# Kernel optimization log

Hardware: AMD Instinct MI355X
Metric: run time of the kernel (lower is better)

## Reference

```python
import jax, jax.numpy as jnp
import numpy as np

N_NODES = 100000
N_EDGES = 3200000
N_FEAT = 128
H = 16
N_CLASSES = 10


def gcn_conv(x, edge_index, W, b, num_nodes):
    """PyG GCNConv (eval): add self-loops, symmetric norm, linear, scatter-add, bias."""
    xw = x @ W  # [N, out]
    loops = jnp.arange(num_nodes, dtype=edge_index.dtype)
    src = jnp.concatenate([edge_index[0], loops])  # message sources (x_j)
    dst = jnp.concatenate([edge_index[1], loops])  # aggregation targets
    ones = jnp.ones(src.shape[0], dtype=xw.dtype)
    deg = jax.ops.segment_sum(ones, dst, num_segments=num_nodes)
    dinv = jnp.where(deg > 0, jax.lax.rsqrt(deg), 0.0)
    norm = dinv[src] * dinv[dst]  # [E+N]
    msg = xw[src] * norm[:, None]  # gather + scale
    out = jax.ops.segment_sum(msg, dst, num_segments=num_nodes)
    return out + b


def setup_inputs() -> dict:
    key = jax.random.key(0)
    ks = jax.random.split(key, 8)
    x = jax.random.normal(ks[0], (N_NODES, N_FEAT), dtype=jnp.float32)
    edge_index = jax.random.randint(ks[1], (2, N_EDGES), 0, N_NODES, dtype=jnp.int64)
    topo_edges = jax.random.randint(ks[2], (2, N_EDGES), 0, N_NODES, dtype=jnp.int64)
    s1 = 1.0 / np.sqrt(N_FEAT)
    s4 = 1.0 / np.sqrt(2 * H)
    W1 = jax.random.normal(ks[3], (N_FEAT, H), dtype=jnp.float32) * s1
    b1 = jnp.zeros((H,), dtype=jnp.float32)
    W2 = jax.random.normal(ks[4], (N_FEAT, H), dtype=jnp.float32) * s1
    b2 = jnp.zeros((H,), dtype=jnp.float32)
    W4 = jax.random.normal(ks[5], (2 * H, N_CLASSES), dtype=jnp.float32) * s4
    b4 = jnp.zeros((N_CLASSES,), dtype=jnp.float32)
    return {"x": x, "edge_index": edge_index, "topo_edges": topo_edges,
            "W1": W1, "b1": b1, "W2": W2, "b2": b2, "W4": W4, "b4": b4}


def reference(x, edge_index, topo_edges, W1, b1, W2, b2, W4, b4):
    n = x.shape[0]
    # branch 1: structural edges
    x1 = jax.nn.relu(gcn_conv(x, edge_index, W1, b1, n))
    # branch 2: topological edges
    x2 = jax.nn.relu(gcn_conv(x, topo_edges, W2, b2, n))
    # dropout is identity in eval mode
    h = jnp.concatenate([x1, x2], axis=1)  # [N, 2H]
    logits = gcn_conv(h, edge_index, W4, b4, n)  # [N, num_classes]
    return jax.nn.log_softmax(logits, axis=1)
```

## Files before the change

kernel.cpp:

```cpp
#include <hip/hip_runtime.h>
#include <hip/hip_fp16.h>

#define N_NODES 100000
#define N_EDGES 3200000
#define NB 1024
#define BW 98
#define SLOT 4096
#define CHUNK 16384


__global__ void k_zero(int* __restrict__ bcur1, int* __restrict__ bcur2) {
    int i = blockIdx.x * blockDim.x + threadIdx.x;
    if (i < NB) { bcur1[i] = 0; bcur2[i] = 0; }
}

__global__ __launch_bounds__(256) void k_part(const int* __restrict__ ei, const int* __restrict__ te,
                                              int* __restrict__ bcur1, int* __restrict__ bcur2,
                                              unsigned* __restrict__ tmp1, unsigned* __restrict__ tmp2,
                                              int E, int PB) {
    extern __shared__ unsigned smem[];
    unsigned* sorted = smem;
    int* loff = (int*)(smem + CHUNK);
    int* rank = loff + NB;
    int* bas  = rank + NB;
    int* ps   = bas + NB;

    int gb = blockIdx.x;
    bool g2 = gb >= PB;
    const int* ed = g2 ? te : ei;
    int* bcur     = g2 ? bcur2 : bcur1;
    unsigned* tmp = g2 ? tmp2 : tmp1;
    int blk = g2 ? gb - PB : gb;
    int t = threadIdx.x;

    for (int i = t; i < NB; i += 256) rank[i] = 0;
    __syncthreads();
    int base = blk * CHUNK, end = min(base + CHUNK, E);
    int csize = end - base;
    for (int e = base + t; e < end; e += 256) atomicAdd(&rank[ed[E + e] / BW], 1);
    __syncthreads();
    int i4 = t * 4;
    int c0 = rank[i4], c1 = rank[i4 + 1], c2 = rank[i4 + 2], c3 = rank[i4 + 3];
    int tot = c0 + c1 + c2 + c3;
    ps[t] = tot;
    __syncthreads();
    #pragma unroll
    for (int d = 1; d < 256; d <<= 1) {
        int a = (t >= d) ? ps[t - d] : 0;
        __syncthreads();
        ps[t] += a;
        __syncthreads();
    }
    int excl = ps[t] - tot;
    loff[i4]     = excl;
    loff[i4 + 1] = excl + c0;
    loff[i4 + 2] = excl + c0 + c1;
    loff[i4 + 3] = excl + c0 + c1 + c2;
    bas[i4]     = c0 ? atomicAdd(&bcur[i4], c0)     : 0;
    bas[i4 + 1] = c1 ? atomicAdd(&bcur[i4 + 1], c1) : 0;
    bas[i4 + 2] = c2 ? atomicAdd(&bcur[i4 + 2], c2) : 0;
    bas[i4 + 3] = c3 ? atomicAdd(&bcur[i4 + 3], c3) : 0;
    rank[i4] = 0; rank[i4 + 1] = 0; rank[i4 + 2] = 0; rank[i4 + 3] = 0;
    __syncthreads();
    for (int e = base + t; e < end; e += 256) {
        int d = ed[E + e], s = ed[e];
        int b = d / BW;
        int r = atomicAdd(&rank[b], 1);
        sorted[loff[b] + r] = ((unsigned)(d - b * BW) << 20) | (unsigned)s;
    }
    __syncthreads();
    for (int i = t; i < csize; i += 256) {
        int lo = 0, hi = NB - 1;
        while (lo < hi) {
            int mid = (lo + hi + 1) >> 1;
            if (loff[mid] <= i) lo = mid; else hi = mid - 1;
        }
        int b = lo;
        int pos = bas[b] + (i - loff[b]);
        if (pos < SLOT) tmp[(size_t)b * SLOT + pos] = sorted[i];
    }
}

__global__ __launch_bounds__(256) void k_csr(const int* __restrict__ bcur1, const int* __restrict__ bcur2,
                                             unsigned* __restrict__ tmp1, unsigned* __restrict__ tmp2,
                                             int2* __restrict__ pk1, int2* __restrict__ pk2,
                                             float* __restrict__ dinv1, float* __restrict__ dinv2, int n) {
    __shared__ unsigned stage[SLOT];
    __shared__ int ncnt[BW], noff[BW], nrank[BW];
    int gb = blockIdx.x;
    bool g2 = gb >= NB;
    int b = g2 ? gb - NB : gb;
    unsigned* tmp = g2 ? tmp2 : tmp1;
    int2* pk      = g2 ? pk2 : pk1;
    float* dinv   = g2 ? dinv2 : dinv1;
    int sz = min((g2 ? bcur2 : bcur1)[b], SLOT);
    int t = threadIdx.x;
    if (t < BW) { ncnt[t] = 0; nrank[t] = 0; }
    __syncthreads();
    size_t base = (size_t)b * SLOT;
    for (int i = t; i < sz; i += 256) {
        unsigned v = tmp[base + i];
        stage[i] = v;
        atomicAdd(&ncnt[v >> 20], 1);
    }
    __syncthreads();
    if (t == 0) {
        int run = 0;
        for (int k = 0; k < BW; ++k) { noff[k] = run; run += ncnt[k]; }
    }
    __syncthreads();
    int nd = b * BW + t;
    if (t < BW && nd < n) {
        pk[nd] = make_int2((int)base + noff[t], ncnt[t]);
        dinv[nd] = rsqrtf((float)ncnt[t] + 1.f);
    }
    for (int i = t; i < sz; i += 256) {
        unsigned v = stage[i];
        int ld = v >> 20;
        int r = atomicAdd(&nrank[ld], 1);
        tmp[base + noff[ld] + r] = v & 0xFFFFFu;
    }
}

__global__ __launch_bounds__(256) void k_gemm12(
    const float* __restrict__ x,
    const float* __restrict__ W1, const float* __restrict__ W2,
    const float* __restrict__ dinv1, const float* __restrict__ dinv2,
    __half* __restrict__ xwh1, __half* __restrict__ xwh2, int n) {
    __shared__ float Wl[128][32];
    __shared__ float xs[8][128];
    int t = threadIdx.x;
    for (int i = t; i < 128 * 16; i += 256) {
        int k = i / 16, o = i % 16;
        Wl[k][o]      = W1[i];
        Wl[k][o + 16] = W2[i];
    }
    int node0 = blockIdx.x * 8;
    for (int i = t; i < 8 * 128; i += 256) {
        int r = i >> 7, c = i & 127;
        int node = node0 + r;
        xs[r][c] = (node < n) ? x[node * 128 + c] : 0.f;
    }
    __syncthreads();
    int r = t >> 5, o = t & 31;
    int node = node0 + r;
    if (node < n) {
        float s = 0.f;
        #pragma unroll
        for (int k = 0; k < 128; ++k) s += xs[r][k] * Wl[k][o];
        if (o < 16) xwh1[(size_t)node * 16 + o]        = __float2half(s * dinv1[node]);
        else        xwh2[(size_t)node * 16 + (o - 16)] = __float2half(s * dinv2[node]);
    }
}

__global__ __launch_bounds__(256) void k_gather12(
    const __half* __restrict__ xwh1, const __half* __restrict__ xwh2,
    const unsigned* __restrict__ csr1, const unsigned* __restrict__ csr2,
    const int2* __restrict__ pk1, const int2* __restrict__ pk2,
    const float* __restrict__ dinv1, const float* __restrict__ dinv2,
    const float* __restrict__ b1, const float* __restrict__ b2,
    __half* __restrict__ h, int n) {
    int t = threadIdx.x;
    int node = blockIdx.x * 8 + (t >> 5);
    int c = t & 31;
    if (node >= n) return;
    bool g1 = (c < 16);
    int cl = g1 ? c : (c - 16);
    const __half* xw    = g1 ? xwh1 : xwh2;
    const unsigned* csr = g1 ? csr1 : csr2;
    int2 oc = g1 ? pk1[node] : pk2[node];
    int o = oc.x, m = oc.y;
    float di = g1 ? dinv1[node] : dinv2[node];
    float acc = __half2float(xw[(size_t)node * 16 + cl]);
    int k = 0;
    for (; k + 4 <= m; k += 4) {
        unsigned j0 = csr[o + k], j1 = csr[o + k + 1], j2 = csr[o + k + 2], j3 = csr[o + k + 3];
        acc += __half2float(xw[(size_t)j0 * 16 + cl]);
        acc += __half2float(xw[(size_t)j1 * 16 + cl]);
        acc += __half2float(xw[(size_t)j2 * 16 + cl]);
        acc += __half2float(xw[(size_t)j3 * 16 + cl]);
    }
    for (; k < m; ++k) acc += __half2float(xw[(size_t)csr[o + k] * 16 + cl]);
    acc *= di;
    float bv = g1 ? b1[cl] : b2[cl];
    float v = acc + bv;
    h[(size_t)node * 32 + c] = __float2half(v > 0.f ? v : 0.f);
}

__global__ void k_gemm3(const __half* __restrict__ h, const float* __restrict__ W4,
                        const float* __restrict__ dinv1, __half* __restrict__ zsh, int n) {
    int i = blockIdx.x * blockDim.x + threadIdx.x;
    if (i >= n) return;
    float hr[32];
    const __half2* hp = (const __half2*)(h + (size_t)i * 32);
    #pragma unroll
    for (int q = 0; q < 16; ++q) {
        float2 f = __half22float2(hp[q]);
        hr[2 * q] = f.x; hr[2 * q + 1] = f.y;
    }
    float di = dinv1[i];
    #pragma unroll
    for (int c = 0; c < 10; ++c) {
        float s = 0.f;
        #pragma unroll
        for (int k = 0; k < 32; ++k) s += hr[k] * W4[k * 10 + c];
        zsh[(size_t)i * 16 + c] = __float2half(s * di);
    }
}

__global__ __launch_bounds__(256) void k_gather3(
    const __half* __restrict__ zsh,
    const unsigned* __restrict__ csr1, const int2* __restrict__ pk1,
    const float* __restrict__ dinv1,
    const float* __restrict__ b4, float* __restrict__ out, int n) {
    int t = threadIdx.x;
    int node = blockIdx.x * 16 + (t >> 4);
    int c = t & 15;
    if (node >= n) return;
    bool act = (c < 10);
    int cc = act ? c : 0;
    float di = dinv1[node];
    float acc = __half2float(zsh[(size_t)node * 16 + cc]);
    int2 oc = pk1[node];
    int o = oc.x, m = oc.y;
    int k = 0;
    for (; k + 4 <= m; k += 4) {
        unsigned j0 = csr1[o + k], j1 = csr1[o + k + 1], j2 = csr1[o + k + 2], j3 = csr1[o + k + 3];
        acc += __half2float(zsh[(size_t)j0 * 16 + cc]);
        acc += __half2float(zsh[(size_t)j1 * 16 + cc]);
        acc += __half2float(zsh[(size_t)j2 * 16 + cc]);
        acc += __half2float(zsh[(size_t)j3 * 16 + cc]);
    }
    for (; k < m; ++k) acc += __half2float(zsh[(size_t)csr1[o + k] * 16 + cc]);
    float logit = acc * di + b4[cc];
    float mv = act ? logit : -1e30f;
    #pragma unroll
    for (int w = 8; w >= 1; w >>= 1) mv = fmaxf(mv, __shfl_xor(mv, w, 16));
    float ex = act ? expf(logit - mv) : 0.f;
    float ssum = ex;
    #pragma unroll
    for (int w = 8; w >= 1; w >>= 1) ssum += __shfl_xor(ssum, w, 16);
    if (act) out[(size_t)node * 10 + c] = logit - mv - logf(ssum);
}

extern "C" void kernel_launch(void* const* d_in, const int* in_sizes, int n_in,
                              void* d_out, int out_size, void* d_ws, size_t ws_size,
                              hipStream_t stream) {
    const float* x  = (const float*)d_in[0];
    const int*   ei = (const int*)d_in[1];
    const int*   te = (const int*)d_in[2];
    const float* W1 = (const float*)d_in[3];
    const float* b1 = (const float*)d_in[4];
    const float* W2 = (const float*)d_in[5];
    const float* b2 = (const float*)d_in[6];
    const float* W4 = (const float*)d_in[7];
    const float* b4 = (const float*)d_in[8];
    float* out = (float*)d_out;

    const int N = N_NODES, E = N_EDGES;

    char* w = (char*)d_ws;
    auto alloc = [&](size_t bytes) { void* p = (void*)w; w += (bytes + 255) & ~255ull; return p; };
    int*      bcur1 = (int*)alloc((size_t)NB * 4);
    int*      bcur2 = (int*)alloc((size_t)NB * 4);
    int2*     pk1   = (int2*)alloc((size_t)N * 8);
    int2*     pk2   = (int2*)alloc((size_t)N * 8);
    float*    dinv1 = (float*)alloc((size_t)N * 4);
    float*    dinv2 = (float*)alloc((size_t)N * 4);
    unsigned* tmp1  = (unsigned*)alloc((size_t)NB * SLOT * 4);
    unsigned* tmp2  = (unsigned*)alloc((size_t)NB * SLOT * 4);
    __half*   xwh1  = (__half*)alloc((size_t)N * 16 * 2);
    __half*   xwh2  = (__half*)alloc((size_t)N * 16 * 2);
    __half*   h     = (__half*)alloc((size_t)N * 32 * 2);
    __half*   zsh   = (__half*)alloc((size_t)N * 16 * 2);

    const int PB = (E + CHUNK - 1) / CHUNK;
    const size_t PART_LDS = ((size_t)CHUNK + 3 * NB + 256) * 4;
    k_zero<<<(NB + 255) / 256, 256, 0, stream>>>(bcur1, bcur2);
    k_part<<<2 * PB, 256, PART_LDS, stream>>>(ei, te, bcur1, bcur2, tmp1, tmp2, E, PB);
    k_csr<<<2 * NB, 256, 0, stream>>>(bcur1, bcur2, tmp1, tmp2, pk1, pk2, dinv1, dinv2, N);
    k_gemm12<<<(N + 7) / 8, 256, 0, stream>>>(x, W1, W2, dinv1, dinv2, xwh1, xwh2, N);
    k_gather12<<<(N + 7) / 8, 256, 0, stream>>>(xwh1, xwh2, tmp1, tmp2, pk1, pk2,
                                                dinv1, dinv2, b1, b2, h, N);
    k_gemm3<<<(N + 255) / 256, 256, 0, stream>>>(h, W4, dinv1, zsh, N);
    k_gather3<<<(N + 15) / 16, 256, 0, stream>>>(zsh, tmp1, pk1, dinv1, b4, out, N);
}
```

Baseline: 426.0 us.

## Replace atomic bucket slots with deterministic per-chunk offset tables and compact CSR

The partition kernel no longer claims bucket positions with global atomics into fixed 4096-entry slots. Each chunk now writes its locally sorted edges contiguously, along with a per-bucket offset table. A new kernel prefix-sums the per-bucket totals to get global bucket bases, and the CSR kernel gathers each bucket's pieces from every chunk into shared memory before building a compact CSR. This removes the global atomics, the per-element binary search and the sparse slotted layout, at the cost of an extra kernel and many small strided reads in the CSR stage. The k_csr gather loop is sized for at most 256 chunks and, like the old SLOT limit, silently drops edges beyond a bucket capacity (now 4608). It also reuses the tmp buffers for the fp16 activations, and the block size changes to 512.

Result: slower. 443.6 us (+4.1%).

```diff
diff --git a/kernel.cpp b/kernel.cpp
--- a/kernel.cpp
+++ b/kernel.cpp
@@ -5,104 +5,134 @@
 #define N_EDGES 3200000
 #define NB 1024
 #define BW 98
-#define SLOT 4096
+#define TBS (NB + 1)
 #define CHUNK 16384
-
-
-__global__ void k_zero(int* __restrict__ bcur1, int* __restrict__ bcur2) {
-    int i = blockIdx.x * blockDim.x + threadIdx.x;
-    if (i < NB) { bcur1[i] = 0; bcur2[i] = 0; }
-}
-
-__global__ __launch_bounds__(256) void k_part(const int* __restrict__ ei, const int* __restrict__ te,
-                                              int* __restrict__ bcur1, int* __restrict__ bcur2,
+#define STCAP 4608
+
+
+__global__ __launch_bounds__(512) void k_part(const int* __restrict__ ei, const int* __restrict__ te,
                                               unsigned* __restrict__ tmp1, unsigned* __restrict__ tmp2,
+                                              unsigned short* __restrict__ tbl1, unsigned short* __restrict__ tbl2,
                                               int E, int PB) {
     extern __shared__ unsigned smem[];
     unsigned* sorted = smem;
-    int* loff = (int*)(smem + CHUNK);
-    int* rank = loff + NB;
-    int* bas  = rank + NB;
-    int* ps   = bas + NB;
+    int* rank = (int*)(smem + CHUNK);
+    int* loff = rank + NB;
+    int* ps   = loff + NB;
 
     int gb = blockIdx.x;
     bool g2 = gb >= PB;
-    const int* ed = g2 ? te : ei;
-    int* bcur     = g2 ? bcur2 : bcur1;
-    unsigned* tmp = g2 ? tmp2 : tmp1;
+    const int* ed        = g2 ? te : ei;
+    unsigned* tmp        = g2 ? tmp2 : tmp1;
+    unsigned short* tbl  = g2 ? tbl2 : tbl1;
     int blk = g2 ? gb - PB : gb;
     int t = threadIdx.x;
 
-    for (int i = t; i < NB; i += 256) rank[i] = 0;
+    for (int i = t; i < NB; i += 512) rank[i] = 0;
     __syncthreads();
     int base = blk * CHUNK, end = min(base + CHUNK, E);
     int csize = end - base;
-    for (int e = base + t; e < end; e += 256) atomicAdd(&rank[ed[E + e] / BW], 1);
-    __syncthreads();
-    int i4 = t * 4;
-    int c0 = rank[i4], c1 = rank[i4 + 1], c2 = rank[i4 + 2], c3 = rank[i4 + 3];
-    int tot = c0 + c1 + c2 + c3;
+    for (int e = base + t; e < end; e += 512) atomicAdd(&rank[ed[E + e] / BW], 1);
+    __syncthreads();
+    int i2 = t * 2;
+    int c0 = rank[i2], c1 = rank[i2 + 1];
+    int tot = c0 + c1;
     ps[t] = tot;
     __syncthreads();
     #pragma unroll
-    for (int d = 1; d < 256; d <<= 1) {
+    for (int d = 1; d < 512; d <<= 1) {
         int a = (t >= d) ? ps[t - d] : 0;
         __syncthreads();
         ps[t] += a;
         __syncthreads();
     }
     int excl = ps[t] - tot;
-    loff[i4]     = excl;
-    loff[i4 + 1] = excl + c0;
-    loff[i4 + 2] = excl + c0 + c1;
-    loff[i4 + 3] = excl + c0 + c1 + c2;
-    bas[i4]     = c0 ? atomicAdd(&bcur[i4], c0)     : 0;
-    bas[i4 + 1] = c1 ? atomicAdd(&bcur[i4 + 1], c1) : 0;
-    bas[i4 + 2] = c2 ? atomicAdd(&bcur[i4 + 2], c2) : 0;
-    bas[i4 + 3] = c3 ? atomicAdd(&bcur[i4 + 3], c3) : 0;
-    rank[i4] = 0; rank[i4 + 1] = 0; rank[i4 + 2] = 0; rank[i4 + 3] = 0;
-    __syncthreads();
-    for (int e = base + t; e < end; e += 256) {
+    loff[i2]     = excl;
+    loff[i2 + 1] = excl + c0;
+    rank[i2] = 0; rank[i2 + 1] = 0;
+    __syncthreads();
+    for (int e = base + t; e < end; e += 512) {
         int d = ed[E + e], s = ed[e];
         int b = d / BW;
         int r = atomicAdd(&rank[b], 1);
         sorted[loff[b] + r] = ((unsigned)(d - b * BW) << 20) | (unsigned)s;
     }
     __syncthreads();
-    for (int i = t; i < csize; i += 256) {
-        int lo = 0, hi = NB - 1;
-        while (lo < hi) {
-            int mid = (lo + hi + 1) >> 1;
-            if (loff[mid] <= i) lo = mid; else hi = mid - 1;
-        }
-        int b = lo;
-        int pos = bas[b] + (i - loff[b]);
-        if (pos < SLOT) tmp[(size_t)b * SLOT + pos] = sorted[i];
-    }
-}
-
-__global__ __launch_bounds__(256) void k_csr(const int* __restrict__ bcur1, const int* __restrict__ bcur2,
-                                             unsigned* __restrict__ tmp1, unsigned* __restrict__ tmp2,
-                                             int2* __restrict__ pk1, int2* __restrict__ pk2,
-                                             float* __restrict__ dinv1, float* __restrict__ dinv2, int n) {
-    __shared__ unsigned stage[SLOT];
+    size_t tb = (size_t)blk * TBS;
+    for (int i = t; i < NB; i += 512) tbl[tb + i] = (unsigned short)loff[i];
+    if (t == 0) tbl[tb + NB] = (unsigned short)csize;
+    size_t ob = (size_t)blk * CHUNK;
+    for (int i = t; i < csize; i += 512) tmp[ob + i] = sorted[i];
+}
+
+__global__ __launch_bounds__(1024) void k_bbase(const unsigned short* __restrict__ tbl1,
+                                                const unsigned short* __restrict__ tbl2,
+                                                int* __restrict__ bbase1, int* __restrict__ bbase2, int PB) {
+    __shared__ int ps[NB];
+    const unsigned short* tbl = blockIdx.x ? tbl2 : tbl1;
+    int* bbase                = blockIdx.x ? bbase2 : bbase1;
+    int b = threadIdx.x;
+    int tot = 0;
+    for (int c = 0; c < PB; ++c) {
+        size_t tb = (size_t)c * TBS;
+        tot += (int)tbl[tb + b + 1] - (int)tbl[tb + b];
+    }
+    ps[b] = tot;
+    __syncthreads();
+    #pragma unroll
+    for (int d = 1; d < NB; d <<= 1) {
+        int a = (b >= d) ? ps[b - d] : 0;
+        __syncthreads();
+        ps[b] += a;
+        __syncthreads();
+    }
+    bbase[b] = ps[b] - tot;
+}
+
+__global__ __launch_bounds__(256) void k_csr(
+    const unsigned* __restrict__ tmp1, const unsigned* __restrict__ tmp2,
+    const unsigned short* __restrict__ tbl1, const unsigned short* __restrict__ tbl2,
+    const int* __restrict__ bbase1, const int* __restrict__ bbase2,
+    unsigned* __restrict__ csr1, unsigned* __restrict__ csr2,
+    int2* __restrict__ pk1, int2* __restrict__ pk2,
+    float* __restrict__ dinv1, float* __restrict__ dinv2, int PB, int n) {
+    __shared__ unsigned stage[STCAP];
     __shared__ int ncnt[BW], noff[BW], nrank[BW];
+    __shared__ int ps[256];
     int gb = blockIdx.x;
     bool g2 = gb >= NB;
     int b = g2 ? gb - NB : gb;
-    unsigned* tmp = g2 ? tmp2 : tmp1;
-    int2* pk      = g2 ? pk2 : pk1;
-    float* dinv   = g2 ? dinv2 : dinv1;
-    int sz = min((g2 ? bcur2 : bcur1)[b], SLOT);
+    const unsigned* tmp       = g2 ? tmp2 : tmp1;
+    const unsigned short* tbl = g2 ? tbl2 : tbl1;
+    unsigned* csr             = g2 ? csr2 : csr1;
+    int2* pk                  = g2 ? pk2 : pk1;
+    float* dinv               = g2 ? dinv2 : dinv1;
+    int bb = (g2 ? bbase2 : bbase1)[b];
     int t = threadIdx.x;
     if (t < BW) { ncnt[t] = 0; nrank[t] = 0; }
-    __syncthreads();
-    size_t base = (size_t)b * SLOT;
-    for (int i = t; i < sz; i += 256) {
-        unsigned v = tmp[base + i];
-        stage[i] = v;
-        atomicAdd(&ncnt[v >> 20], 1);
-    }
+    int start = 0, len = 0;
+    if (t < PB) {
+        size_t tb = (size_t)t * TBS;
+        start = tbl[tb + b];
+        len = (int)tbl[tb + b + 1] - start;
+    }
+    ps[t] = len;
+    __syncthreads();
+    #pragma unroll
+    for (int d = 1; d < 256; d <<= 1) {
+        int a = (t >= d) ? ps[t - d] : 0;
+        __syncthreads();
+        ps[t] += a;
+        __syncthreads();
+    }
+    int ofs = ps[t] - len;
+    int sz = min(ps[255], STCAP);
+    for (int i = 0; i < len; ++i) {
+        int p = ofs + i;
+        if (p < STCAP) stage[p] = tmp[(size_t)t * CHUNK + start + i];
+    }
+    __syncthreads();
+    for (int i = t; i < sz; i += 256) atomicAdd(&ncnt[stage[i] >> 20], 1);
     __syncthreads();
     if (t == 0) {
         int run = 0;
@@ -111,14 +141,14 @@
     __syncthreads();
     int nd = b * BW + t;
     if (t < BW && nd < n) {
-        pk[nd] = make_int2((int)base + noff[t], ncnt[t]);
+        pk[nd] = make_int2(bb + noff[t], ncnt[t]);
         dinv[nd] = rsqrtf((float)ncnt[t] + 1.f);
     }
     for (int i = t; i < sz; i += 256) {
         unsigned v = stage[i];
         int ld = v >> 20;
         int r = atomicAdd(&nrank[ld], 1);
-        tmp[base + noff[ld] + r] = v & 0xFFFFFu;
+        csr[bb + noff[ld] + r] = v & 0xFFFFFu;
     }
 }
 
@@ -258,30 +288,35 @@
     float* out = (float*)d_out;
 
     const int N = N_NODES, E = N_EDGES;
+    const int PB = (E + CHUNK - 1) / CHUNK;
 
     char* w = (char*)d_ws;
     auto alloc = [&](size_t bytes) { void* p = (void*)w; w += (bytes + 255) & ~255ull; return p; };
-    int*      bcur1 = (int*)alloc((size_t)NB * 4);
-    int*      bcur2 = (int*)alloc((size_t)NB * 4);
-    int2*     pk1   = (int2*)alloc((size_t)N * 8);
-    int2*     pk2   = (int2*)alloc((size_t)N * 8);
-    float*    dinv1 = (float*)alloc((size_t)N * 4);
-    float*    dinv2 = (float*)alloc((size_t)N * 4);
-    unsigned* tmp1  = (unsigned*)alloc((size_t)NB * SLOT * 4);
-    unsigned* tmp2  = (unsigned*)alloc((size_t)NB * SLOT * 4);
-    __half*   xwh1  = (__half*)alloc((size_t)N * 16 * 2);
-    __half*   xwh2  = (__half*)alloc((size_t)N * 16 * 2);
-    __half*   h     = (__half*)alloc((size_t)N * 32 * 2);
-    __half*   zsh   = (__half*)alloc((size_t)N * 16 * 2);
-
-    const int PB = (E + CHUNK - 1) / CHUNK;
-    const size_t PART_LDS = ((size_t)CHUNK + 3 * NB + 256) * 4;
-    k_zero<<<(NB + 255) / 256, 256, 0, stream>>>(bcur1, bcur2);
-    k_part<<<2 * PB, 256, PART_LDS, stream>>>(ei, te, bcur1, bcur2, tmp1, tmp2, E, PB);
-    k_csr<<<2 * NB, 256, 0, stream>>>(bcur1, bcur2, tmp1, tmp2, pk1, pk2, dinv1, dinv2, N);
+    unsigned* tmp1 = (unsigned*)alloc((size_t)PB * CHUNK * 4);
+    unsigned* tmp2 = (unsigned*)alloc((size_t)PB * CHUNK * 4);
+    unsigned* csr1 = (unsigned*)alloc((size_t)E * 4);
+    unsigned* csr2 = (unsigned*)alloc((size_t)E * 4);
+    unsigned short* tbl1 = (unsigned short*)alloc((size_t)PB * TBS * 2);
+    unsigned short* tbl2 = (unsigned short*)alloc((size_t)PB * TBS * 2);
+    int*   bbase1 = (int*)alloc((size_t)NB * 4);
+    int*   bbase2 = (int*)alloc((size_t)NB * 4);
+    int2*  pk1    = (int2*)alloc((size_t)N * 8);
+    int2*  pk2    = (int2*)alloc((size_t)N * 8);
+    float* dinv1  = (float*)alloc((size_t)N * 4);
+    float* dinv2  = (float*)alloc((size_t)N * 4);
+    __half* xwh1 = (__half*)tmp1;
+    __half* xwh2 = xwh1 + (size_t)N * 16;
+    __half* h    = xwh2 + (size_t)N * 16;
+    __half* zsh  = h + (size_t)N * 32;
+
+    const size_t PART_LDS = ((size_t)CHUNK + 2 * NB + 512) * 4;
+    k_part<<<2 * PB, 512, PART_LDS, stream>>>(ei, te, tmp1, tmp2, tbl1, tbl2, E, PB);
+    k_bbase<<<2, 1024, 0, stream>>>(tbl1, tbl2, bbase1, bbase2, PB);
+    k_csr<<<2 * NB, 256, 0, stream>>>(tmp1, tmp2, tbl1, tbl2, bbase1, bbase2,
+                                      csr1, csr2, pk1, pk2, dinv1, dinv2, PB, N);
     k_gemm12<<<(N + 7) / 8, 256, 0, stream>>>(x, W1, W2, dinv1, dinv2, xwh1, xwh2, N);
-    k_gather12<<<(N + 7) / 8, 256, 0, stream>>>(xwh1, xwh2, tmp1, tmp2, pk1, pk2,
+    k_gather12<<<(N + 7) / 8, 256, 0, stream>>>(xwh1, xwh2, csr1, csr2, pk1, pk2,
                                                 dinv1, dinv2, b1, b2, h, N);
     k_gemm3<<<(N + 255) / 256, 256, 0, stream>>>(h, W4, dinv1, zsh, N);
-    k_gather3<<<(N + 15) / 16, 256, 0, stream>>>(zsh, tmp1, pk1, dinv1, b4, out, N);
-}
+    k_gather3<<<(N + 15) / 16, 256, 0, stream>>>(zsh, csr1, pk1, dinv1, b4, out, N);
+}
```
